# Kernel tuning notes

Measured on AMD Instinct MI355X. Metric: run time of the kernel, lower is better.

The kernel has to match this reference:

```python
import jax, jax.numpy as jnp
import numpy as np

B, N, D, T = 32, 512, 128, 8
NEG_SLOPE = 0.2
MASK_VAL = -1e10


def _xavier(key, shape, gain=1.0):
    fan_in, fan_out = shape[0], int(np.prod(shape[1:]))
    limit = gain * np.sqrt(6.0 / (fan_in + fan_out))
    return jax.random.uniform(key, shape, jnp.float32, -limit, limit)


def setup_inputs() -> dict:
    key = jax.random.key(0)
    ks = jax.random.split(key, 8)
    atom_embeddings = jax.random.normal(ks[0], (B, N, D), dtype=jnp.float32)
    # bond types in [-1, T-1]; -1 = no bond (masked)
    edges = jax.random.randint(ks[1], (B, N, N), 0, T + 1, dtype=jnp.int64) - 1
    Qw = _xavier(ks[2], (D, D))
    Kw = _xavier(ks[3], (D, D))
    Vw = _xavier(ks[4], (D, D))
    Pw = _xavier(ks[5], (D, D))
    Qb = jnp.zeros((D,), jnp.float32)
    Kb = jnp.zeros((D,), jnp.float32)
    Vb = jnp.zeros((D,), jnp.float32)
    Pb = jnp.zeros((D,), jnp.float32)
    a = _xavier(ks[6], (D, D, T), gain=1.414)
    return {"atom_embeddings": atom_embeddings, "edges": edges,
            "Qw": Qw, "Qb": Qb, "Kw": Kw, "Kb": Kb, "Vw": Vw, "Vb": Vb,
            "a": a, "Pw": Pw, "Pb": Pb}


def reference(atom_embeddings, edges, Qw, Qb, Kw, Kb, Vw, Vb, a, Pw, Pb):
    # torch Linear: x @ W.T + b
    src = atom_embeddings @ Qw.T + Qb            # (B,N,D)
    dst = atom_embeddings @ Kw.T + Kb            # (B,N,D)
    val = atom_embeddings @ Vw.T + Vb            # (B,N,D)

    # bilinear edge-type scores: s[b,n,m,t] = src[b,n,:] @ a[:,:,t] @ dst[b,m,:]
    ts = jnp.einsum('bnd,det->bnet', src, a)     # (B,N,D,T)
    scores = jnp.einsum('bnet,bme->bnmt', ts, dst)  # (B,N,N,T)

    # gather the slice for each edge's bond type (clamp -1 -> 0 like torch)
    idx = jnp.clip(edges, 0, None)[..., None]    # (B,N,N,1)
    att = jnp.take_along_axis(scores, idx, axis=-1)[..., 0]  # (B,N,N)
    att = jnp.where(edges == -1, MASK_VAL, att)
    att = jnp.where(att >= 0, att, NEG_SLOPE * att)  # leaky_relu
    att = jax.nn.softmax(att, axis=-1)           # (B,N,N)

    out = att @ val                              # (B,N,D)
    return out @ Pw.T + Pb
```

## Files before the change

kernel.cpp:

```cpp
#include <hip/hip_runtime.h>
#include <stdint.h>


typedef short bf16x8 __attribute__((ext_vector_type(8)));
typedef float f32x4 __attribute__((ext_vector_type(4)));
typedef unsigned short u16;
typedef unsigned int u32;
typedef unsigned long long u64;

__device__ __forceinline__ u16 f2bf(float x) {
    union { float f; u32 u; } v; v.f = x;
    u32 r = v.u + 0x7FFFu + ((v.u >> 16) & 1u);
    return (u16)(r >> 16);
}
__device__ __forceinline__ float bf2f(u16 h) {
    union { u32 u; float f; } v; v.u = ((u32)h) << 16; return v.f;
}
__device__ __forceinline__ void split_hl(float x, u16& h, u16& l) {
    h = f2bf(x);
    l = f2bf(x - bf2f(h));
}
__device__ __forceinline__ void split4(float4 x, u64& hq, u64& lq) {
    u16 h0, l0, h1, l1, h2, l2, h3, l3;
    split_hl(x.x, h0, l0); split_hl(x.y, h1, l1);
    split_hl(x.z, h2, l2); split_hl(x.w, h3, l3);
    hq = (u64)h0 | ((u64)h1 << 16) | ((u64)h2 << 32) | ((u64)h3 << 48);
    lq = (u64)l0 | ((u64)l1 << 16) | ((u64)l2 << 32) | ((u64)l3 << 48);
}
__device__ __forceinline__ void split8(float4 a, float4 b, bf16x8& h8, bf16x8& l8) {
    u16 hh[8], ll[8];
    split_hl(a.x, hh[0], ll[0]); split_hl(a.y, hh[1], ll[1]);
    split_hl(a.z, hh[2], ll[2]); split_hl(a.w, hh[3], ll[3]);
    split_hl(b.x, hh[4], ll[4]); split_hl(b.y, hh[5], ll[5]);
    split_hl(b.z, hh[6], ll[6]); split_hl(b.w, hh[7], ll[7]);
    #pragma unroll
    for (int i = 0; i < 8; i++) { h8[i] = (short)hh[i]; l8[i] = (short)ll[i]; }
}
__device__ __forceinline__ f32x4 mfma16(bf16x8 a, bf16x8 b, f32x4 c) {
    return __builtin_amdgcn_mfma_f32_16x16x32_bf16(a, b, c, 0, 0, 0);
}

__global__ void prep_kernel(const float* __restrict__ Qw, const float* __restrict__ Qb,
                            const float* __restrict__ Kw, const float* __restrict__ Kb,
                            const float* __restrict__ Vw, const float* __restrict__ Vb,
                            const float* __restrict__ Aa, const float* __restrict__ Pw,
                            u16* __restrict__ WFH, u16* __restrict__ WFL,
                            float* __restrict__ bcat) {
    int gid = blockIdx.x * 256 + threadIdx.x;
    if (gid >= 1280 * 32) return;
    int j = gid >> 5, dq = gid & 31;
    int d4 = dq * 4;
    float4 v = {0.f, 0.f, 0.f, 0.f};
    float bias = 0.f;
    if (j < 128) {
        v = *(const float4*)(Kw + j * 128 + d4);
        bias = Kb[j];
    } else if (j < 256) {
        int jj = j - 128;
        for (int k = 0; k < 128; k++) {
            float p = Pw[jj * 128 + k];
            float4 w = *(const float4*)(Vw + k * 128 + d4);
            v.x += p * w.x; v.y += p * w.y; v.z += p * w.z; v.w += p * w.w;
            bias += p * Vb[k];
        }
    } else {
        int r = j - 256, t = r >> 7, jj = r & 127;
        for (int e = 0; e < 128; e++) {
            float av = Aa[(e * 128 + jj) * 8 + t];
            float4 w = *(const float4*)(Qw + e * 128 + d4);
            v.x += av * w.x; v.y += av * w.y; v.z += av * w.z; v.w += av * w.w;
            bias += Qb[e] * av;
        }
    }
    u64 hq, lq; split4(v, hq, lq);
    size_t base = ((size_t)((j >> 4) * 16 + (dq >> 1)) * 16 + (j & 15)) * 8 + (dq & 1) * 4;
    *(u64*)(WFH + base) = hq;
    *(u64*)(WFL + base) = lq;
    if (dq == 0) bcat[j] = bias;
}

__global__ void detect_kernel(const int* __restrict__ E, int* __restrict__ flag) {
    __shared__ int bad;
    if (threadIdx.x == 0) bad = 0;
    __syncthreads();
    int w0 = E[2 * threadIdx.x + 1];
    int w1 = E[2 * (threadIdx.x + 256) + 1];
    if (!(w0 == 0 || w0 == -1) || !(w1 == 0 || w1 == -1)) atomicOr(&bad, 1);
    __syncthreads();
    if (threadIdx.x == 0) *flag = (bad ? 0 : 1);
}

__launch_bounds__(256, 4)
__global__ void gemm1_kernel(const float* __restrict__ X,
                             const u16* __restrict__ WFH, const u16* __restrict__ WFL,
                             const float* __restrict__ bcat,
                             u16* __restrict__ FSH, u16* __restrict__ FSL,
                             u16* __restrict__ FBH, u16* __restrict__ FBL,
                             u16* __restrict__ VFH, u16* __restrict__ VFL) {
    const int id = blockIdx.x;
    const int xcd = id & 7, q = id >> 3;
    const int g0 = (xcd * 32 + (q >> 2)) * 64;
    const int jsplit = q & 3;
    const int tid = threadIdx.x;
    const int wid = tid >> 6, lane = tid & 63;
    const int gblk = (wid >> 1) * 32, jblk = (wid & 1) * 32;
    const int lr = lane & 15, lg = lane >> 4;

    bf16x8 afh[4][2], afl[4][2];
    #pragma unroll
    for (int ks = 0; ks < 4; ks++)
    #pragma unroll
    for (int r = 0; r < 2; r++) {
        const float* p = X + (size_t)(g0 + gblk + r * 16 + lr) * 128 + ks * 32 + lg * 8;
        float4 a = *(const float4*)p;
        float4 b = *(const float4*)(p + 4);
        split8(a, b, afh[ks][r], afl[ks][r]);
    }
    const int b = g0 >> 9;

    #pragma unroll
    for (int jt5 = 0; jt5 < 5; jt5++) {
        const int jt = jsplit * 5 + jt5;
        const int j0 = jt * 64;
        const bool valTile = (jt == 2 || jt == 3);
        const int jgbase = (j0 + jblk) >> 4;
        f32x4 acc[2][2] = {};
        if (valTile) {
            #pragma unroll
            for (int ks = 0; ks < 4; ks++) {
                bf16x8 bfh[2], bfl[2];
                #pragma unroll
                for (int c = 0; c < 2; c++) {
                    size_t eo = ((size_t)((jgbase + c) * 16 + ks * 4 + lg) * 16 + lr) * 8;
                    bfh[c] = *(const bf16x8*)(WFH + eo);
                    bfl[c] = *(const bf16x8*)(WFL + eo);
                }
                #pragma unroll
                for (int r = 0; r < 2; r++)
                #pragma unroll
                for (int c = 0; c < 2; c++) {
                    acc[r][c] = mfma16(afh[ks][r], bfh[c], acc[r][c]);
                    acc[r][c] = mfma16(afh[ks][r], bfl[c], acc[r][c]);
                    acc[r][c] = mfma16(afl[ks][r], bfh[c], acc[r][c]);
                }
            }
            #pragma unroll
            for (int r = 0; r < 2; r++)
            #pragma unroll
            for (int c = 0; c < 2; c++) {
                int j = j0 + jblk + c * 16 + lr;
                float bias = bcat[j];
                int d = j - 128;
                int mbase = (g0 & 511) + gblk + r * 16 + 4 * lg;
                float4 v = {acc[r][c][0] + bias, acc[r][c][1] + bias,
                            acc[r][c][2] + bias, acc[r][c][3] + bias};
                u64 hq, lq; split4(v, hq, lq);
                int kc = mbase >> 3;
                size_t off = ((size_t)(b * 64 + kc) * 128 + d) * 8 + (mbase & 7);
                *(u64*)(VFH + off) = hq;
                *(u64*)(VFL + off) = lq;
            }
        } else {
            #pragma unroll
            for (int ks = 0; ks < 4; ks++) {
                bf16x8 bfh[2], bfl[2];
                #pragma unroll
                for (int c = 0; c < 2; c++) {
                    size_t eo = ((size_t)((jgbase + c) * 16 + ks * 4 + lg) * 16 + lr) * 8;
                    bfh[c] = *(const bf16x8*)(WFH + eo);
                    bfl[c] = *(const bf16x8*)(WFL + eo);
                }
                #pragma unroll
                for (int c = 0; c < 2; c++)
                #pragma unroll
                for (int r = 0; r < 2; r++) {
                    acc[c][r] = mfma16(bfh[c], afh[ks][r], acc[c][r]);
                    acc[c][r] = mfma16(bfh[c], afl[ks][r], acc[c][r]);
                    acc[c][r] = mfma16(bfl[c], afh[ks][r], acc[c][r]);
                }
            }
            if (jt < 2) {
                const int mt = (g0 & 511) >> 7;
                const int mbase = g0 & 127;
                size_t fb = (size_t)(b * 4 + mt) * 16384;
                #pragma unroll
                for (int c = 0; c < 2; c++)
                #pragma unroll
                for (int r = 0; r < 2; r++) {
                    int d0 = j0 + jblk + c * 16 + 4 * lg;
                    float4 bias4 = *(const float4*)(bcat + d0);
                    float4 v = {acc[c][r][0] + bias4.x, acc[c][r][1] + bias4.y,
                                acc[c][r][2] + bias4.z, acc[c][r][3] + bias4.w};
                    u64 hq, lq; split4(v, hq, lq);
                    int kc = (d0 >> 5) * 4 + ((d0 >> 3) & 3);
                    int mrow = mbase + gblk + r * 16 + lr;
                    size_t off = fb + ((size_t)kc * 128 + mrow) * 8 + (d0 & 7);
                    *(u64*)(FBH + off) = hq;
                    *(u64*)(FBL + off) = lq;
                }
            } else {
                const int nt = (g0 & 511) >> 6;
                const int tt = (jt - 4) >> 1;
                size_t fs = ((size_t)(b * 8 + nt) * 8 + tt) * 8192;
                #pragma unroll
                for (int c = 0; c < 2; c++)
                #pragma unroll
                for (int r = 0; r < 2; r++) {
                    int j = j0 + jblk + c * 16 + 4 * lg;
                    float4 bias4 = *(const float4*)(bcat + j);
                    float4 v = {acc[c][r][0] + bias4.x, acc[c][r][1] + bias4.y,
                                acc[c][r][2] + bias4.z, acc[c][r][3] + bias4.w};
                    u64 hq, lq; split4(v, hq, lq);
                    int d0 = ((jt - 4) & 1) * 64 + jblk + c * 16 + 4 * lg;
                    int kc = (d0 >> 5) * 4 + ((d0 >> 3) & 3);
                    int nrow = gblk + r * 16 + lr;
                    size_t off = fs + ((size_t)kc * 64 + nrow) * 8 + (d0 & 7);
                    *(u64*)(FSH + off) = hq;
                    *(u64*)(FSL + off) = lq;
                }
            }
        }
    }
}

__launch_bounds__(256, 2)
__global__ void scores_kernel(const u16* __restrict__ FSH, const u16* __restrict__ FSL,
                              const u16* __restrict__ FBH, const u16* __restrict__ FBL,
                              const void* __restrict__ Eptr, const int* __restrict__ flag,
                              float* __restrict__ att) {
    const int id = blockIdx.x;
    const int xcd = id & 7, s = id >> 3;
    const int b = xcd * 4 + (s >> 6);
    const int tile = s & 63;
    const int n0 = (tile >> 3) * 64, m0 = (tile & 7) * 64;
    const int nt = n0 >> 6;
    const int mt = m0 >> 7, mb = m0 & 127;
    const int tid = threadIdx.x;
    const int wid = tid >> 6, lane = tid & 63;
    const int wr = (wid >> 1) * 32, wc = (wid & 1) * 32;
    const int lr = lane & 15, lg = lane >> 4;
    const bool e64 = (*flag != 0);
    const int estride = e64 ? 2 : 1;

    u32 edpk[2][2];
    u32 mneg = 0;
    #pragma unroll
    for (int r = 0; r < 2; r++)
    #pragma unroll
    for (int c = 0; c < 2; c++) {
        u32 pk = 0;
        #pragma unroll
        for (int q = 0; q < 4; q++) {
            size_t n = n0 + wr + r * 16 + 4 * lg + q;
            size_t m = m0 + wc + c * 16 + lr;
            size_t idx = ((size_t)b * 512 + n) * 512 + m;
            int e = ((const int*)Eptr)[idx * estride];
            pk |= (u32)(e & 0xff) << (q * 8);
            if (e < 0) mneg |= 1u << (r * 8 + c * 4 + q);
        }
        edpk[r][c] = pk;
    }

    bf16x8 bfh[4][2], bfl[4][2];
    #pragma unroll
    for (int ks = 0; ks < 4; ks++)
    #pragma unroll
    for (int c = 0; c < 2; c++) {
        size_t eo = (size_t)(b * 4 + mt) * 16384
                  + ((size_t)((ks * 4 + lg) * 128 + mb + wc + c * 16 + lr)) * 8;
        bfh[ks][c] = *(const bf16x8*)(FBH + eo);
        bfl[ks][c] = *(const bf16x8*)(FBL + eo);
    }
    float sel[2][2][4];
    #pragma unroll
    for (int r = 0; r < 2; r++)
    #pragma unroll
    for (int c = 0; c < 2; c++)
    #pragma unroll
    for (int q = 0; q < 4; q++) sel[r][c][q] = 0.f;

    const size_t abase0 = (size_t)(b * 8 + nt) * 8 * 8192
                        + (size_t)(lg * 64) * 8;

    #pragma unroll 1
    for (int t = 0; t < 8; t++) {
        const size_t abase = abase0 + (size_t)t * 8192;
        bf16x8 afh[4][2], afl[4][2];
        #pragma unroll
        for (int ks = 0; ks < 4; ks++)
        #pragma unroll
        for (int r = 0; r < 2; r++) {
            size_t eo = abase + (size_t)(ks * 4 * 64 + wr + r * 16 + lr) * 8;
            afh[ks][r] = *(const bf16x8*)(FSH + eo);
            afl[ks][r] = *(const bf16x8*)(FSL + eo);
        }
        __builtin_amdgcn_sched_barrier(0);
        f32x4 acc[2][2] = {};
        #pragma unroll
        for (int ks = 0; ks < 4; ks++) {
            #pragma unroll
            for (int r = 0; r < 2; r++)
            #pragma unroll
            for (int c = 0; c < 2; c++) {
                acc[r][c] = mfma16(afh[ks][r], bfh[ks][c], acc[r][c]);
                acc[r][c] = mfma16(afh[ks][r], bfl[ks][c], acc[r][c]);
                acc[r][c] = mfma16(afl[ks][r], bfh[ks][c], acc[r][c]);
            }
        }
        #pragma unroll
        for (int r = 0; r < 2; r++)
        #pragma unroll
        for (int c = 0; c < 2; c++) {
            u32 x = edpk[r][c];
            #pragma unroll
            for (int q = 0; q < 4; q++) {
                bool hit = ((x >> (q * 8)) & 0xffu) == (u32)t;
                sel[r][c][q] = hit ? acc[r][c][q] : sel[r][c][q];
            }
        }
    }
    #pragma unroll
    for (int r = 0; r < 2; r++)
    #pragma unroll
    for (int c = 0; c < 2; c++)
    #pragma unroll
    for (int q = 0; q < 4; q++) {
        bool neg = (mneg >> (r * 8 + c * 4 + q)) & 1;
        float v = neg ? -1e10f : sel[r][c][q];
        v = (v >= 0.f) ? v : 0.2f * v;
        size_t n = n0 + wr + r * 16 + 4 * lg + q;
        size_t m = m0 + wc + c * 16 + lr;
        att[((size_t)b * 512 + n) * 512 + m] = v;
    }
}

__launch_bounds__(256, 3)
__global__ void out_kernel(const float* __restrict__ att,
                           const u16* __restrict__ VFH, const u16* __restrict__ VFL,
                           const float* __restrict__ Pb, float* __restrict__ out) {
    const int id = blockIdx.x;
    const int xcd = id & 7, j = id >> 3;
    const int b = xcd * 4 + (j >> 4);
    const int n0 = (j & 15) * 32;
    __shared__ u16 PH[2][32 * 64], PL[2][32 * 64];
    const int tid = threadIdx.x;
    const int row = tid >> 3, c8 = tid & 7;
    const float* rp = att + ((size_t)b * 512 + n0 + row) * 512 + c8 * 8;

    float mx = -1e30f;
    #pragma unroll
    for (int mc = 0; mc < 8; mc++) {
        float4 a0 = *(const float4*)(rp + mc * 64);
        float4 a1 = *(const float4*)(rp + mc * 64 + 4);
        mx = fmaxf(mx, fmaxf(fmaxf(fmaxf(a0.x, a0.y), fmaxf(a0.z, a0.w)),
                             fmaxf(fmaxf(a1.x, a1.y), fmaxf(a1.z, a1.w))));
    }
    #pragma unroll
    for (int o = 1; o < 8; o <<= 1) mx = fmaxf(mx, __shfl_xor(mx, o, 64));
    float s = 0.f;
    #pragma unroll
    for (int mc = 0; mc < 8; mc++) {
        float4 a0 = *(const float4*)(rp + mc * 64);
        float4 a1 = *(const float4*)(rp + mc * 64 + 4);
        s += expf(a0.x - mx) + expf(a0.y - mx) + expf(a0.z - mx) + expf(a0.w - mx)
           + expf(a1.x - mx) + expf(a1.y - mx) + expf(a1.z - mx) + expf(a1.w - mx);
    }
    #pragma unroll
    for (int o = 1; o < 8; o <<= 1) s += __shfl_xor(s, o, 64);
    const float inv = 1.0f / s;

    const int wid = tid >> 6, lane = tid & 63;
    const int lr = lane & 15, lg = lane >> 4;
    const int wc = wid * 32;
    const int pboff = (row * 128 + c8 * 16) ^ ((row & 7) << 4);

    {
        float4 a0 = *(const float4*)(rp);
        float4 a1 = *(const float4*)(rp + 4);
        float4 p0 = {expf(a0.x - mx) * inv, expf(a0.y - mx) * inv,
                     expf(a0.z - mx) * inv, expf(a0.w - mx) * inv};
        float4 p1 = {expf(a1.x - mx) * inv, expf(a1.y - mx) * inv,
                     expf(a1.z - mx) * inv, expf(a1.w - mx) * inv};
        u64 h0, l0, h1, l1;
        split4(p0, h0, l0); split4(p1, h1, l1);
        *(u64*)((char*)PH[0] + pboff) = h0;
        *(u64*)((char*)PH[0] + pboff + 8) = h1;
        *(u64*)((char*)PL[0] + pboff) = l0;
        *(u64*)((char*)PL[0] + pboff + 8) = l1;
    }
    f32x4 acc[2][2] = {};
    for (int mc = 0; mc < 8; mc++) {
        __syncthreads();
        if (mc < 7) {
            float4 a0 = *(const float4*)(rp + (mc + 1) * 64);
            float4 a1 = *(const float4*)(rp + (mc + 1) * 64 + 4);
            float4 p0 = {expf(a0.x - mx) * inv, expf(a0.y - mx) * inv,
                         expf(a0.z - mx) * inv, expf(a0.w - mx) * inv};
            float4 p1 = {expf(a1.x - mx) * inv, expf(a1.y - mx) * inv,
                         expf(a1.z - mx) * inv, expf(a1.w - mx) * inv};
            u64 h0, l0, h1, l1;
            split4(p0, h0, l0); split4(p1, h1, l1);
            int nb = (mc + 1) & 1;
            *(u64*)((char*)PH[nb] + pboff) = h0;
            *(u64*)((char*)PH[nb] + pboff + 8) = h1;
            *(u64*)((char*)PL[nb] + pboff) = l0;
            *(u64*)((char*)PL[nb] + pboff + 8) = l1;
        }
        bf16x8 vh[2][2], vl[2][2];
        #pragma unroll
        for (int ks = 0; ks < 2; ks++)
        #pragma unroll
        for (int c = 0; c < 2; c++) {
            int kc = mc * 8 + ks * 4 + lg;
            size_t eo = ((size_t)(b * 64 + kc) * 128 + wc + c * 16 + lr) * 8;
            vh[ks][c] = *(const bf16x8*)(VFH + eo);
            vl[ks][c] = *(const bf16x8*)(VFL + eo);
        }
        __builtin_amdgcn_sched_barrier(0);
        const int cur = mc & 1;
        #pragma unroll
        for (int ks = 0; ks < 2; ks++) {
            const int kb2 = (ks * 32 + lg * 8) * 2;
            bf16x8 ah[2], al[2];
            #pragma unroll
            for (int r = 0; r < 2; r++) {
                int prow = r * 16 + lr;
                int boff = (prow * 128 + kb2) ^ ((prow & 7) << 4);
                ah[r] = *(const bf16x8*)((const char*)PH[cur] + boff);
                al[r] = *(const bf16x8*)((const char*)PL[cur] + boff);
            }
            #pragma unroll
            for (int c = 0; c < 2; c++)
            #pragma unroll
            for (int r = 0; r < 2; r++) {
                acc[r][c] = mfma16(ah[r], vh[ks][c], acc[r][c]);
                acc[r][c] = mfma16(ah[r], vl[ks][c], acc[r][c]);
                acc[r][c] = mfma16(al[r], vh[ks][c], acc[r][c]);
            }
        }
    }
    #pragma unroll
    for (int r = 0; r < 2; r++)
    #pragma unroll
    for (int c = 0; c < 2; c++)
    #pragma unroll
    for (int q = 0; q < 4; q++) {
        int n = n0 + r * 16 + 4 * lg + q;
        int d = wc + c * 16 + lr;
        out[((size_t)b * 512 + n) * 128 + d] = acc[r][c][q] + Pb[d];
    }
}

extern "C" void kernel_launch(void* const* d_in, const int* in_sizes, int n_in,
                              void* d_out, int out_size, void* d_ws, size_t ws_size,
                              hipStream_t stream) {
    (void)in_sizes; (void)n_in; (void)out_size; (void)ws_size;
    const float* X  = (const float*)d_in[0];
    const void*  E  = d_in[1];
    const float* Qw = (const float*)d_in[2];
    const float* Qb = (const float*)d_in[3];
    const float* Kw = (const float*)d_in[4];
    const float* Kb = (const float*)d_in[5];
    const float* Vw = (const float*)d_in[6];
    const float* Vb = (const float*)d_in[7];
    const float* Aa = (const float*)d_in[8];
    const float* Pw = (const float*)d_in[9];
    const float* Pb = (const float*)d_in[10];
    float* out = (float*)d_out;

    char* ws = (char*)d_ws;
    size_t cur = 0;
    auto alloc = [&](size_t bytes) -> char* {
        char* p = ws + cur;
        cur += (bytes + 255) & ~(size_t)255;
        return p;
    };
    int*   flag = (int*)  alloc(4);
    u16*   WFH  = (u16*)  alloc((size_t)1280 * 128 * 2);
    u16*   WFL  = (u16*)  alloc((size_t)1280 * 128 * 2);
    float* bcat = (float*)alloc(1280 * 4);
    u16*   FSH  = (u16*)  alloc((size_t)32 * 8 * 8 * 8192 * 2);
    u16*   FSL  = (u16*)  alloc((size_t)32 * 8 * 8 * 8192 * 2);
    u16*   FBH  = (u16*)  alloc((size_t)32 * 4 * 16384 * 2);
    u16*   FBL  = (u16*)  alloc((size_t)32 * 4 * 16384 * 2);
    u16*   VFH  = (u16*)  alloc((size_t)32 * 64 * 128 * 8 * 2);
    u16*   VFL  = (u16*)  alloc((size_t)32 * 64 * 128 * 8 * 2);
    float* att  = (float*)alloc((size_t)32 * 512 * 512 * 4);

    prep_kernel<<<160, 256, 0, stream>>>(Qw, Qb, Kw, Kb, Vw, Vb, Aa, Pw, WFH, WFL, bcat);
    detect_kernel<<<1, 256, 0, stream>>>((const int*)E, flag);
    gemm1_kernel<<<1024, 256, 0, stream>>>(X, WFH, WFL, bcat, FSH, FSL, FBH, FBL, VFH, VFL);
    scores_kernel<<<2048, 256, 0, stream>>>(FSH, FSL, FBH, FBL, E, flag, att);
    out_kernel<<<512, 256, 0, stream>>>(att, VFH, VFL, Pb, out);
}
```

Before: 228.2 us.

## Double-buffer A-fragment loads in score kernel and cache att rows in registers

The bond-type loop in the score kernel is software-pipelined with two register buffers, so the A-fragment loads for type t+1 (and t+2) are issued while the MFMAs for type t run, hiding global-load latency. In the output kernel each thread loads its attention row slice into registers once and reuses it for the max, the exp-sum and the probability writes. This replaces three global reads and two expf evaluations per element with one read and one expf. The extra registers force launch bounds down from 3 to 2 blocks per SM, which lowers occupancy.

```diff
diff --git a/kernel.cpp b/kernel.cpp
--- a/kernel.cpp
+++ b/kernel.cpp
@@ -282,43 +282,62 @@
     const size_t abase0 = (size_t)(b * 8 + nt) * 8 * 8192
                         + (size_t)(lg * 64) * 8;
 
+    bf16x8 a0h[4][2], a0l[4][2], a1h[4][2], a1l[4][2];
+
+#define LOAD_A(AH_, AL_, T_)                                                   \
+    {                                                                          \
+        const size_t ab_ = abase0 + (size_t)(T_) * 8192;                       \
+        _Pragma("unroll")                                                      \
+        for (int ks = 0; ks < 4; ks++)                                         \
+        _Pragma("unroll")                                                      \
+        for (int r = 0; r < 2; r++) {                                          \
+            size_t eo = ab_ + (size_t)(ks * 4 * 64 + wr + r * 16 + lr) * 8;    \
+            AH_[ks][r] = *(const bf16x8*)(FSH + eo);                           \
+            AL_[ks][r] = *(const bf16x8*)(FSL + eo);                           \
+        }                                                                      \
+    }
+
+#define COMPUTE_T(AH_, AL_, T_)                                                \
+    {                                                                          \
+        f32x4 acc[2][2] = {};                                                  \
+        _Pragma("unroll")                                                      \
+        for (int ks = 0; ks < 4; ks++) {                                       \
+            _Pragma("unroll")                                                  \
+            for (int r = 0; r < 2; r++)                                        \
+            _Pragma("unroll")                                                  \
+            for (int c = 0; c < 2; c++) {                                      \
+                acc[r][c] = mfma16(AH_[ks][r], bfh[ks][c], acc[r][c]);         \
+                acc[r][c] = mfma16(AH_[ks][r], bfl[ks][c], acc[r][c]);         \
+                acc[r][c] = mfma16(AL_[ks][r], bfh[ks][c], acc[r][c]);         \
+            }                                                                  \
+        }                                                                      \
+        _Pragma("unroll")                                                      \
+        for (int r = 0; r < 2; r++)                                            \
+        _Pragma("unroll")                                                      \
+        for (int c = 0; c < 2; c++) {                                          \
+            u32 x = edpk[r][c];                                                \
+            _Pragma("unroll")                                                  \
+            for (int q = 0; q < 4; q++) {                                      \
+                bool hit = ((x >> (q * 8)) & 0xffu) == (u32)(T_);              \
+                sel[r][c][q] = hit ? acc[r][c][q] : sel[r][c][q];              \
+            }                                                                  \
+        }                                                                      \
+    }
+
+    LOAD_A(a0h, a0l, 0);
     #pragma unroll 1
-    for (int t = 0; t < 8; t++) {
-        const size_t abase = abase0 + (size_t)t * 8192;
-        bf16x8 afh[4][2], afl[4][2];
-        #pragma unroll
-        for (int ks = 0; ks < 4; ks++)
-        #pragma unroll
-        for (int r = 0; r < 2; r++) {
-            size_t eo = abase + (size_t)(ks * 4 * 64 + wr + r * 16 + lr) * 8;
-            afh[ks][r] = *(const bf16x8*)(FSH + eo);
-            afl[ks][r] = *(const bf16x8*)(FSL + eo);
-        }
+    for (int tp = 0; tp < 4; tp++) {
+        const int t = tp * 2;
+        LOAD_A(a1h, a1l, t + 1);
         __builtin_amdgcn_sched_barrier(0);
-        f32x4 acc[2][2] = {};
-        #pragma unroll
-        for (int ks = 0; ks < 4; ks++) {
-            #pragma unroll
-            for (int r = 0; r < 2; r++)
-            #pragma unroll
-            for (int c = 0; c < 2; c++) {
-                acc[r][c] = mfma16(afh[ks][r], bfh[ks][c], acc[r][c]);
-                acc[r][c] = mfma16(afh[ks][r], bfl[ks][c], acc[r][c]);
-                acc[r][c] = mfma16(afl[ks][r], bfh[ks][c], acc[r][c]);
-            }
-        }
-        #pragma unroll
-        for (int r = 0; r < 2; r++)
-        #pragma unroll
-        for (int c = 0; c < 2; c++) {
-            u32 x = edpk[r][c];
-            #pragma unroll
-            for (int q = 0; q < 4; q++) {
-                bool hit = ((x >> (q * 8)) & 0xffu) == (u32)t;
-                sel[r][c][q] = hit ? acc[r][c][q] : sel[r][c][q];
-            }
-        }
-    }
+        COMPUTE_T(a0h, a0l, t);
+        if (tp < 3) LOAD_A(a0h, a0l, t + 2);
+        __builtin_amdgcn_sched_barrier(0);
+        COMPUTE_T(a1h, a1l, t + 1);
+    }
+#undef LOAD_A
+#undef COMPUTE_T
+
     #pragma unroll
     for (int r = 0; r < 2; r++)
     #pragma unroll
@@ -334,7 +353,7 @@
     }
 }
 
-__launch_bounds__(256, 3)
+__launch_bounds__(256, 2)
 __global__ void out_kernel(const float* __restrict__ att,
                            const u16* __restrict__ VFH, const u16* __restrict__ VFL,
                            const float* __restrict__ Pb, float* __restrict__ out) {
@@ -347,23 +366,29 @@
     const int row = tid >> 3, c8 = tid & 7;
     const float* rp = att + ((size_t)b * 512 + n0 + row) * 512 + c8 * 8;
 
+    float4 av0[8], av1[8];
+    #pragma unroll
+    for (int mc = 0; mc < 8; mc++) {
+        av0[mc] = *(const float4*)(rp + mc * 64);
+        av1[mc] = *(const float4*)(rp + mc * 64 + 4);
+    }
     float mx = -1e30f;
     #pragma unroll
     for (int mc = 0; mc < 8; mc++) {
-        float4 a0 = *(const float4*)(rp + mc * 64);
-        float4 a1 = *(const float4*)(rp + mc * 64 + 4);
-        mx = fmaxf(mx, fmaxf(fmaxf(fmaxf(a0.x, a0.y), fmaxf(a0.z, a0.w)),
-                             fmaxf(fmaxf(a1.x, a1.y), fmaxf(a1.z, a1.w))));
+        mx = fmaxf(mx, fmaxf(fmaxf(fmaxf(av0[mc].x, av0[mc].y), fmaxf(av0[mc].z, av0[mc].w)),
+                             fmaxf(fmaxf(av1[mc].x, av1[mc].y), fmaxf(av1[mc].z, av1[mc].w))));
     }
     #pragma unroll
     for (int o = 1; o < 8; o <<= 1) mx = fmaxf(mx, __shfl_xor(mx, o, 64));
     float s = 0.f;
     #pragma unroll
     for (int mc = 0; mc < 8; mc++) {
-        float4 a0 = *(const float4*)(rp + mc * 64);
-        float4 a1 = *(const float4*)(rp + mc * 64 + 4);
-        s += expf(a0.x - mx) + expf(a0.y - mx) + expf(a0.z - mx) + expf(a0.w - mx)
-           + expf(a1.x - mx) + expf(a1.y - mx) + expf(a1.z - mx) + expf(a1.w - mx);
+        av0[mc].x = expf(av0[mc].x - mx); av0[mc].y = expf(av0[mc].y - mx);
+        av0[mc].z = expf(av0[mc].z - mx); av0[mc].w = expf(av0[mc].w - mx);
+        av1[mc].x = expf(av1[mc].x - mx); av1[mc].y = expf(av1[mc].y - mx);
+        av1[mc].z = expf(av1[mc].z - mx); av1[mc].w = expf(av1[mc].w - mx);
+        s += av0[mc].x + av0[mc].y + av0[mc].z + av0[mc].w
+           + av1[mc].x + av1[mc].y + av1[mc].z + av1[mc].w;
     }
     #pragma unroll
     for (int o = 1; o < 8; o <<= 1) s += __shfl_xor(s, o, 64);
@@ -375,12 +400,8 @@
     const int pboff = (row * 128 + c8 * 16) ^ ((row & 7) << 4);
 
     {
-        float4 a0 = *(const float4*)(rp);
-        float4 a1 = *(const float4*)(rp + 4);
-        float4 p0 = {expf(a0.x - mx) * inv, expf(a0.y - mx) * inv,
-                     expf(a0.z - mx) * inv, expf(a0.w - mx) * inv};
-        float4 p1 = {expf(a1.x - mx) * inv, expf(a1.y - mx) * inv,
-                     expf(a1.z - mx) * inv, expf(a1.w - mx) * inv};
+        float4 p0 = {av0[0].x * inv, av0[0].y * inv, av0[0].z * inv, av0[0].w * inv};
+        float4 p1 = {av1[0].x * inv, av1[0].y * inv, av1[0].z * inv, av1[0].w * inv};
         u64 h0, l0, h1, l1;
         split4(p0, h0, l0); split4(p1, h1, l1);
         *(u64*)((char*)PH[0] + pboff) = h0;
@@ -389,15 +410,14 @@
         *(u64*)((char*)PL[0] + pboff + 8) = l1;
     }
     f32x4 acc[2][2] = {};
+    #pragma unroll
     for (int mc = 0; mc < 8; mc++) {
         __syncthreads();
         if (mc < 7) {
-            float4 a0 = *(const float4*)(rp + (mc + 1) * 64);
-            float4 a1 = *(const float4*)(rp + (mc + 1) * 64 + 4);
-            float4 p0 = {expf(a0.x - mx) * inv, expf(a0.y - mx) * inv,
-                         expf(a0.z - mx) * inv, expf(a0.w - mx) * inv};
-            float4 p1 = {expf(a1.x - mx) * inv, expf(a1.y - mx) * inv,
-                         expf(a1.z - mx) * inv, expf(a1.w - mx) * inv};
+            float4 p0 = {av0[mc + 1].x * inv, av0[mc + 1].y * inv,
+                         av0[mc + 1].z * inv, av0[mc + 1].w * inv};
+            float4 p1 = {av1[mc + 1].x * inv, av1[mc + 1].y * inv,
+                         av1[mc + 1].z * inv, av1[mc + 1].w * inv};
             u64 h0, l0, h1, l1;
             split4(p0, h0, l0); split4(p1, h1, l1);
             int nb = (mc + 1) & 1;
```

Result: slower. 410.2 us (+79.7%).
